# Kernel optimization log

Measured on AMD Instinct MI355X. Metric: run time of the kernel, lower is better.

## Reference

```python
import jax, jax.numpy as jnp
import numpy as np

NUM_HEADS = 12
HIDDEN = 768
HEAD_DIM = HIDDEN // NUM_HEADS  # 64
B, S = 2, 2048


def setup_inputs() -> dict:
    key = jax.random.key(0)
    ks = jax.random.split(key, 8)
    inp = {
        "hidden_states": jax.random.normal(ks[0], (B, S, HIDDEN), dtype=jnp.float32),
        "attention_mask": jnp.zeros((B, 1, 1, S), dtype=jnp.float32),
        "Wq": jax.random.normal(ks[1], (HIDDEN, HIDDEN), dtype=jnp.float32) * 0.02,
        "bq": jnp.zeros((HIDDEN,), dtype=jnp.float32),
        "Wk": jax.random.normal(ks[2], (HIDDEN, HIDDEN), dtype=jnp.float32) * 0.02,
        "bk": jnp.zeros((HIDDEN,), dtype=jnp.float32),
        "Wv": jax.random.normal(ks[3], (HIDDEN, HIDDEN), dtype=jnp.float32) * 0.02,
        "bv": jnp.zeros((HIDDEN,), dtype=jnp.float32),
    }
    return inp


def _split_heads(x):
    # [B, S, H*d] -> [B, H, S, d]
    b, s, _ = x.shape
    return x.reshape(b, s, NUM_HEADS, HEAD_DIM).transpose(0, 2, 1, 3)


def reference(hidden_states, attention_mask, Wq, bq, Wk, bk, Wv, bv):
    # Q/K/V projections (nn.Linear: x @ W.T + b; W generated square so direct matmul is equivalent math)
    q = _split_heads(hidden_states @ Wq + bq)  # [B,H,S,d]
    k = _split_heads(hidden_states @ Wk + bk)
    v = _split_heads(hidden_states @ Wv + bv)

    scale = 1.0 / np.sqrt(HEAD_DIM).astype(np.float32)
    scores = jnp.einsum("bhqd,bhkd->bhqk", q, k) * scale  # [B,H,S,S]
    scores = scores + attention_mask  # additive mask, broadcast [B,1,1,S]
    probs = jax.nn.softmax(scores, axis=-1)
    # dropout prob = 0.0 -> identity (eval mode)
    ctx = jnp.einsum("bhqk,bhkd->bhqd", probs, v)  # [B,H,S,d]
    ctx = ctx.transpose(0, 2, 1, 3).reshape(hidden_states.shape[0], hidden_states.shape[1], HIDDEN)
    return ctx
```

## Files before the change

### kernel.cpp

```cpp
#include <hip/hip_runtime.h>

#define S_LEN 2048
#define HID   768
#define NH    12
#define HD    64
#define BATCH 2
#define GK    768
#define L2E   1.44269504088896340736f
#define QSCL  (0.125f * L2E)

typedef __attribute__((ext_vector_type(8))) short bf16x8;
typedef __attribute__((ext_vector_type(4))) float f32x4;
typedef __attribute__((ext_vector_type(4))) short s16x4;
typedef __attribute__((ext_vector_type(8))) short s16x8;

__device__ __forceinline__ unsigned short f2bf(float f) {
    union { float f; unsigned int u; } v; v.f = f;
    unsigned int r = v.u + 0x7fffu + ((v.u >> 16) & 1u);
    return (unsigned short)(r >> 16);
}
__device__ __forceinline__ unsigned short f2bf_hu(float f) {
    union { float f; unsigned int u; } v; v.f = f;
    return (unsigned short)((v.u + 0x8000u) >> 16);
}

#define GLL16(gp, lp) __builtin_amdgcn_global_load_lds( \
    (const __attribute__((address_space(1))) unsigned int*)(gp), \
    (__attribute__((address_space(3))) unsigned int*)(lp), 16, 0, 0)


__global__ __launch_bounds__(256) void prep_kernel(
    const float* __restrict__ X, const float* __restrict__ Wq,
    const float* __restrict__ Wk, const float* __restrict__ Wv,
    unsigned short* __restrict__ Xb, unsigned short* __restrict__ Wt) {
    __shared__ float T[32][33];
    int bid = blockIdx.x;
    if (bid < 3072) {
        int id = bid * 256 + threadIdx.x;
        float4 v = ((const float4*)X)[id];
        s16x4 o; o[0] = (short)f2bf(v.x); o[1] = (short)f2bf(v.y);
        o[2] = (short)f2bf(v.z); o[3] = (short)f2bf(v.w);
        ((s16x4*)Xb)[id] = o;
        return;
    }
    int t2 = bid - 3072;
    int mat = t2 / 576, t = t2 % 576;
    int tk = t / 24, tn = t % 24;
    const float* W = (mat == 0) ? Wq : (mat == 1) ? Wk : Wv;
    const float scl = (mat == 0) ? QSCL : 1.0f;
    int r  = threadIdx.x >> 3;
    int c4 = (threadIdx.x & 7) * 4;
    float4 v = *(const float4*)&W[(size_t)(tk*32 + r) * GK + tn*32 + c4];
    T[c4+0][r] = v.x; T[c4+1][r] = v.y; T[c4+2][r] = v.z; T[c4+3][r] = v.w;
    __syncthreads();
    s16x4 o;
    o[0] = (short)f2bf(T[r][c4+0] * scl); o[1] = (short)f2bf(T[r][c4+1] * scl);
    o[2] = (short)f2bf(T[r][c4+2] * scl); o[3] = (short)f2bf(T[r][c4+3] * scl);
    *(s16x4*)&Wt[(size_t)(mat*768 + tn*32 + r) * GK + tk*32 + c4] = o;
}

__global__ __launch_bounds__(256) void gemm_qkv(
    const unsigned short* __restrict__ Xb, const unsigned short* __restrict__ Wt,
    const float* __restrict__ bq, const float* __restrict__ bk,
    const float* __restrict__ bv,
    unsigned short* __restrict__ qb, unsigned short* __restrict__ kb,
    unsigned short* __restrict__ vb) {
    __shared__ __align__(16) unsigned short As[2][128][64];
    __shared__ __align__(16) unsigned short Bs[2][64][64];

    const int tid = threadIdx.x;
    const int bm = blockIdx.y * 128;
    const int bn = blockIdx.x * 64;
    const int w = tid >> 6, l = tid & 63, quad = l >> 4, lq = l & 15;
    const int wx = w & 1, wy = w >> 1;

    const int srow = l >> 3, schunk = ((l & 7) ^ (l >> 3)) * 8;
    const unsigned short* aga = Xb + (size_t)(bm + w*32 + srow) * GK + schunk;
    const unsigned short* bga = Wt + (size_t)(bn + w*16 + srow) * GK + schunk;

    const int c0 = ((quad)     ^ (lq & 7)) * 8;
    const int c1 = ((4 + quad) ^ (lq & 7)) * 8;

    f32x4 zero = {0.f, 0.f, 0.f, 0.f};
    f32x4 acc[4][2];
#pragma unroll
    for (int mi = 0; mi < 4; mi++)
#pragma unroll
        for (int ni = 0; ni < 2; ni++) acc[mi][ni] = zero;

    auto stage = [&](int buf, int ks) {
        const int k0 = ks * 64;
#pragma unroll
        for (int i = 0; i < 4; i++)
            GLL16(aga + k0 + i*8*GK, &As[buf][w*32 + i*8][0]);
#pragma unroll
        for (int i = 0; i < 2; i++)
            GLL16(bga + k0 + i*8*GK, &Bs[buf][w*16 + i*8][0]);
    };

    auto compute = [&](int buf) {
#pragma unroll
        for (int kh = 0; kh < 2; kh++) {
            const int cc = kh ? c1 : c0;
            bf16x8 a[4], b[2];
#pragma unroll
            for (int mi = 0; mi < 4; mi++)
                a[mi] = *(const bf16x8*)&As[buf][wy*64 + mi*16 + lq][cc];
#pragma unroll
            for (int ni = 0; ni < 2; ni++)
                b[ni] = *(const bf16x8*)&Bs[buf][wx*32 + ni*16 + lq][cc];
#pragma unroll
            for (int mi = 0; mi < 4; mi++)
#pragma unroll
                for (int ni = 0; ni < 2; ni++)
                    acc[mi][ni] = __builtin_amdgcn_mfma_f32_16x16x32_bf16(
                        a[mi], b[ni], acc[mi][ni], 0, 0, 0);
        }
    };

    stage(0, 0);
    __syncthreads();
    for (int ks = 0; ks < GK / 64; ks += 2) {
        stage(1, ks + 1);
        compute(0);
        __syncthreads();
        if (ks + 2 < GK / 64) stage(0, ks + 2);
        compute(1);
        __syncthreads();
    }

    unsigned short* ep = (unsigned short*)As;
    const int mat = bn / 768;
    const float* bias = (mat == 0) ? bq : (mat == 1) ? bk : bv;
    const float bscl = (mat == 0) ? QSCL : 1.0f;
    const int nbase = bn % 768;
    const int h  = nbase >> 6;
    const int b_ = bm >> 11, s0 = bm & 2047;

    if (mat != 1) {
#pragma unroll
        for (int ni = 0; ni < 2; ni++) {
            int nl = wx*32 + ni*16 + lq;
            float bval = bias[nbase + nl] * bscl;
#pragma unroll
            for (int mi = 0; mi < 4; mi++) {
                int m0 = wy*64 + mi*16 + quad*4;
                s16x4 pk;
#pragma unroll
                for (int r = 0; r < 4; r++) pk[r] = (short)f2bf_hu(acc[mi][ni][r] + bval);
                *(s16x4*)&ep[nl*136 + m0] = pk;
            }
        }
        __syncthreads();
        unsigned short* outp = (mat == 0) ? qb : vb;
        unsigned short* obase = outp + ((size_t)((b_*NH + h) * HD)) * S_LEN + s0;
#pragma unroll
        for (int i = 0; i < 4; i++) {
            int id = i * 256 + tid;
            int n = id >> 4, c = id & 15;
            *(s16x8*)&obase[(size_t)n * S_LEN + c*8] = *(const s16x8*)&ep[n*136 + c*8];
        }
    } else {
#pragma unroll
        for (int ni = 0; ni < 2; ni++) {
            int nl = wx*32 + ni*16 + lq;
            float bval = bias[nbase + nl];
#pragma unroll
            for (int mi = 0; mi < 4; mi++) {
                int m0 = wy*64 + mi*16 + quad*4;
#pragma unroll
                for (int r = 0; r < 4; r++)
                    ep[(m0 + r)*66 + nl] = f2bf_hu(acc[mi][ni][r] + bval);
            }
        }
        __syncthreads();
        unsigned short* obase = kb + ((size_t)((b_*NH + h) * S_LEN + s0)) * HD;
#pragma unroll
        for (int i = 0; i < 4; i++) {
            int id = i * 256 + tid;
            int m = id >> 3, c = id & 7;
            *(s16x8*)&obase[(size_t)m * HD + c*8] = *(const s16x8*)&ep[m*66 + c*8];
        }
    }
}

__global__ __launch_bounds__(256) void attn_kernel(
    const unsigned short* __restrict__ Qtg, const unsigned short* __restrict__ Kg,
    const unsigned short* __restrict__ Vtg, const float* __restrict__ maskg,
    float* __restrict__ out) {
    __shared__ __align__(16) unsigned short Ks[2][64][64];
    __shared__ __align__(16) unsigned short Vt[2][64][64];
    __shared__ __align__(16) unsigned short Ps[4][16][72];
    __shared__ __align__(16) float mkL[S_LEN];

    const int tid = threadIdx.x;
    const int w = tid >> 6, l = tid & 63, quad = l >> 4, lq = l & 15;
    const int bh = blockIdx.y;
    const int q0 = blockIdx.x * 64;
    const int bi = bh / NH, hi = bh % NH;
    const unsigned short* Kh = Kg + (size_t)bh * S_LEN * HD;
    const unsigned short* Vh = Vtg + (size_t)bh * HD * S_LEN;

    bf16x8 a0, a1;
    {
        const unsigned short* Qt = Qtg + (size_t)bh * HD * S_LEN + (q0 + w*16 + lq);
#pragma unroll
        for (int j = 0; j < 8; j++) {
            a0[j] = (short)Qt[(size_t)(quad*8 + j) * S_LEN];
            a1[j] = (short)Qt[(size_t)(quad*8 + j + 32) * S_LEN];
        }
    }

    {
        const float4* mb4 = (const float4*)(maskg + (size_t)bi * S_LEN);
#pragma unroll
        for (int i = 0; i < 2; i++) {
            int idx = i * 256 + tid;
            float4 v = mb4[idx];
            float4 sv; sv.x = v.x*L2E; sv.y = v.y*L2E; sv.z = v.z*L2E; sv.w = v.w*L2E;
            ((float4*)mkL)[idx] = sv;
        }
    }

    bf16x8 ones;
#pragma unroll
    for (int i = 0; i < 8; i++) ones[i] = (short)0x3F80;

    const int srow = l >> 3, schunk = ((l & 7) ^ (l >> 3)) * 8;
    const unsigned short* kga = Kh + (size_t)(w*16 + srow) * HD + schunk;
    const unsigned short* vga = Vh + (size_t)(w*16 + srow) * S_LEN + schunk;

    const int c0 = ((quad)     ^ (lq & 7)) * 8;
    const int c1 = ((4 + quad) ^ (lq & 7)) * 8;

    f32x4 zero = {0.f, 0.f, 0.f, 0.f};
    f32x4 o[4], lsum = zero;
#pragma unroll
    for (int ng = 0; ng < 4; ng++) o[ng] = zero;

    auto stage = [&](int buf, int kt) {
#pragma unroll
        for (int i = 0; i < 2; i++) {
            GLL16(kga + (size_t)kt*64*HD + i*8*HD, &Ks[buf][w*16 + i*8][0]);
            GLL16(vga + kt*64 + (size_t)i*8*S_LEN, &Vt[buf][w*16 + i*8][0]);
        }
    };

    auto compute = [&](int buf, int kt) {
        const int kk = kt * 64;
        float mm[4];
#pragma unroll
        for (int g = 0; g < 4; g++) mm[g] = mkL[kk + g*16 + lq];

        f32x4 s[4];
#pragma unroll
        for (int g = 0; g < 4; g++) {
            bf16x8 b0 = *(const bf16x8*)&Ks[buf][g*16 + lq][c0];
            bf16x8 b1 = *(const bf16x8*)&Ks[buf][g*16 + lq][c1];
            f32x4 z = __builtin_amdgcn_mfma_f32_16x16x32_bf16(a0, b0, zero, 0, 0, 0);
            s[g]    = __builtin_amdgcn_mfma_f32_16x16x32_bf16(a1, b1, z,    0, 0, 0);
        }

#pragma unroll
        for (int g = 0; g < 4; g++) {
            const int col = g*16 + lq;
#pragma unroll
            for (int r = 0; r < 4; r++)
                Ps[w][quad*4 + r][col] = f2bf_hu(exp2f(s[g][r] + mm[g]));
        }

        bf16x8 pa0 = *(const bf16x8*)&Ps[w][lq][quad*8];
        bf16x8 pa1 = *(const bf16x8*)&Ps[w][lq][32 + quad*8];

        lsum = __builtin_amdgcn_mfma_f32_16x16x32_bf16(pa0, ones, lsum, 0, 0, 0);
        lsum = __builtin_amdgcn_mfma_f32_16x16x32_bf16(pa1, ones, lsum, 0, 0, 0);

#pragma unroll
        for (int ng = 0; ng < 4; ng++) {
            bf16x8 v0 = *(const bf16x8*)&Vt[buf][ng*16 + lq][c0];
            bf16x8 v1 = *(const bf16x8*)&Vt[buf][ng*16 + lq][c1];
            f32x4 t = __builtin_amdgcn_mfma_f32_16x16x32_bf16(pa0, v0, o[ng], 0, 0, 0);
            o[ng]   = __builtin_amdgcn_mfma_f32_16x16x32_bf16(pa1, v1, t,     0, 0, 0);
        }
    };

    stage(0, 0);
    __syncthreads();

    for (int kt = 0; kt < S_LEN / 64; kt += 2) {
        stage(1, kt + 1);
        compute(0, kt);
        __syncthreads();
        if (kt + 2 < S_LEN / 64) stage(0, kt + 2);
        compute(1, kt + 1);
        __syncthreads();
    }

#pragma unroll
    for (int r = 0; r < 4; r++) {
        const float inv = 1.0f / lsum[r];
        const int row = q0 + w*16 + quad*4 + r;
#pragma unroll
        for (int ng = 0; ng < 4; ng++)
            out[((size_t)(bi * S_LEN + row)) * HID + hi*HD + ng*16 + lq] = o[ng][r] * inv;
    }
}

extern "C" void kernel_launch(void* const* d_in, const int* in_sizes, int n_in,
                              void* d_out, int out_size, void* d_ws, size_t ws_size,
                              hipStream_t stream) {
    const float* X    = (const float*)d_in[0];
    const float* mask = (const float*)d_in[1];
    const float* Wq   = (const float*)d_in[2];
    const float* bq   = (const float*)d_in[3];
    const float* Wk   = (const float*)d_in[4];
    const float* bk   = (const float*)d_in[5];
    const float* Wv   = (const float*)d_in[6];
    const float* bv   = (const float*)d_in[7];
    float* out = (float*)d_out;

    const size_t per = (size_t)BATCH * NH * S_LEN * HD;
    unsigned short* qb = (unsigned short*)d_ws;
    unsigned short* kb = qb + per;
    unsigned short* vb = kb + per;
    unsigned short* xb = vb + per;
    unsigned short* wt = xb + (size_t)4096 * GK;

    prep_kernel<<<4800, 256, 0, stream>>>(X, Wq, Wk, Wv, xb, wt);

    dim3 ggrid(2304 / 64, 4096 / 128);
    gemm_qkv<<<ggrid, 256, 0, stream>>>(xb, wt, bq, bk, bv, qb, kb, vb);

    dim3 agrid(S_LEN / 64, BATCH * NH);
    attn_kernel<<<agrid, 256, 0, stream>>>(qb, kb, vb, mask, out);
}
```

Before: 162.3 us.

## Switch bf16 to fp16 MFMA with packed conversions and transpose grid order

Replaces the bf16 data path with fp16 throughout. Conversions now use hardware packed round-toward-zero cvt_pkrtz or native half casts instead of integer bit manipulation, which cuts ALU work in the prep, GEMM epilogue and softmax P-store code. Separately, both the GEMM and attention grids are transposed so that consecutive blocks walk a different dimension, changing L2 reuse of weights and K/V across concurrently scheduled blocks. fp16 has a narrower exponent range than bf16, so exp2 values or projections with large magnitude could overflow.

Result: no change. 164.2 us (+1.2%).

```diff
diff --git a/kernel.cpp b/kernel.cpp
--- a/kernel.cpp
+++ b/kernel.cpp
@@ -9,19 +9,19 @@
 #define L2E   1.44269504088896340736f
 #define QSCL  (0.125f * L2E)
 
-typedef __attribute__((ext_vector_type(8))) short bf16x8;
+typedef __attribute__((ext_vector_type(8))) _Float16 f16x8;
+typedef __attribute__((ext_vector_type(2))) __fp16 fp16v2;
 typedef __attribute__((ext_vector_type(4))) float f32x4;
 typedef __attribute__((ext_vector_type(4))) short s16x4;
 typedef __attribute__((ext_vector_type(8))) short s16x8;
 
-__device__ __forceinline__ unsigned short f2bf(float f) {
-    union { float f; unsigned int u; } v; v.f = f;
-    unsigned int r = v.u + 0x7fffu + ((v.u >> 16) & 1u);
-    return (unsigned short)(r >> 16);
-}
-__device__ __forceinline__ unsigned short f2bf_hu(float f) {
-    union { float f; unsigned int u; } v; v.f = f;
-    return (unsigned short)((v.u + 0x8000u) >> 16);
+__device__ __forceinline__ unsigned short f2h(float f) {
+    _Float16 h = (_Float16)f;
+    union { _Float16 h; unsigned short u; } v; v.h = h; return v.u;
+}
+__device__ __forceinline__ unsigned int pkh(float a, float b) {
+    fp16v2 r = __builtin_amdgcn_cvt_pkrtz(a, b);
+    union { fp16v2 h; unsigned int u; } v; v.h = r; return v.u;
 }
 
 #define GLL16(gp, lp) __builtin_amdgcn_global_load_lds( \
@@ -38,9 +38,8 @@
     if (bid < 3072) {
         int id = bid * 256 + threadIdx.x;
         float4 v = ((const float4*)X)[id];
-        s16x4 o; o[0] = (short)f2bf(v.x); o[1] = (short)f2bf(v.y);
-        o[2] = (short)f2bf(v.z); o[3] = (short)f2bf(v.w);
-        ((s16x4*)Xb)[id] = o;
+        uint2 u; u.x = pkh(v.x, v.y); u.y = pkh(v.z, v.w);
+        ((uint2*)Xb)[id] = u;
         return;
     }
     int t2 = bid - 3072;
@@ -53,10 +52,10 @@
     float4 v = *(const float4*)&W[(size_t)(tk*32 + r) * GK + tn*32 + c4];
     T[c4+0][r] = v.x; T[c4+1][r] = v.y; T[c4+2][r] = v.z; T[c4+3][r] = v.w;
     __syncthreads();
-    s16x4 o;
-    o[0] = (short)f2bf(T[r][c4+0] * scl); o[1] = (short)f2bf(T[r][c4+1] * scl);
-    o[2] = (short)f2bf(T[r][c4+2] * scl); o[3] = (short)f2bf(T[r][c4+3] * scl);
-    *(s16x4*)&Wt[(size_t)(mat*768 + tn*32 + r) * GK + tk*32 + c4] = o;
+    uint2 u;
+    u.x = pkh(T[r][c4+0] * scl, T[r][c4+1] * scl);
+    u.y = pkh(T[r][c4+2] * scl, T[r][c4+3] * scl);
+    *(uint2*)&Wt[(size_t)(mat*768 + tn*32 + r) * GK + tk*32 + c4] = u;
 }
 
 __global__ __launch_bounds__(256) void gemm_qkv(
@@ -69,8 +68,8 @@
     __shared__ __align__(16) unsigned short Bs[2][64][64];
 
     const int tid = threadIdx.x;
-    const int bm = blockIdx.y * 128;
-    const int bn = blockIdx.x * 64;
+    const int bm = blockIdx.x * 128;
+    const int bn = blockIdx.y * 64;
     const int w = tid >> 6, l = tid & 63, quad = l >> 4, lq = l & 15;
     const int wx = w & 1, wy = w >> 1;
 
@@ -102,18 +101,18 @@
 #pragma unroll
         for (int kh = 0; kh < 2; kh++) {
             const int cc = kh ? c1 : c0;
-            bf16x8 a[4], b[2];
+            f16x8 a[4], b[2];
 #pragma unroll
             for (int mi = 0; mi < 4; mi++)
-                a[mi] = *(const bf16x8*)&As[buf][wy*64 + mi*16 + lq][cc];
+                a[mi] = *(const f16x8*)&As[buf][wy*64 + mi*16 + lq][cc];
 #pragma unroll
             for (int ni = 0; ni < 2; ni++)
-                b[ni] = *(const bf16x8*)&Bs[buf][wx*32 + ni*16 + lq][cc];
+                b[ni] = *(const f16x8*)&Bs[buf][wx*32 + ni*16 + lq][cc];
 #pragma unroll
             for (int mi = 0; mi < 4; mi++)
 #pragma unroll
                 for (int ni = 0; ni < 2; ni++)
-                    acc[mi][ni] = __builtin_amdgcn_mfma_f32_16x16x32_bf16(
+                    acc[mi][ni] = __builtin_amdgcn_mfma_f32_16x16x32_f16(
                         a[mi], b[ni], acc[mi][ni], 0, 0, 0);
         }
     };
@@ -145,10 +144,10 @@
 #pragma unroll
             for (int mi = 0; mi < 4; mi++) {
                 int m0 = wy*64 + mi*16 + quad*4;
-                s16x4 pk;
-#pragma unroll
-                for (int r = 0; r < 4; r++) pk[r] = (short)f2bf_hu(acc[mi][ni][r] + bval);
-                *(s16x4*)&ep[nl*136 + m0] = pk;
+                uint2 u;
+                u.x = pkh(acc[mi][ni][0] + bval, acc[mi][ni][1] + bval);
+                u.y = pkh(acc[mi][ni][2] + bval, acc[mi][ni][3] + bval);
+                *(uint2*)&ep[nl*136 + m0] = u;
             }
         }
         __syncthreads();
@@ -170,7 +169,7 @@
                 int m0 = wy*64 + mi*16 + quad*4;
 #pragma unroll
                 for (int r = 0; r < 4; r++)
-                    ep[(m0 + r)*66 + nl] = f2bf_hu(acc[mi][ni][r] + bval);
+                    ep[(m0 + r)*66 + nl] = f2h(acc[mi][ni][r] + bval);
             }
         }
         __syncthreads();
@@ -195,21 +194,22 @@
 
     const int tid = threadIdx.x;
     const int w = tid >> 6, l = tid & 63, quad = l >> 4, lq = l & 15;
-    const int bh = blockIdx.y;
-    const int q0 = blockIdx.x * 64;
+    const int bh = blockIdx.x;
+    const int q0 = blockIdx.y * 64;
     const int bi = bh / NH, hi = bh % NH;
     const unsigned short* Kh = Kg + (size_t)bh * S_LEN * HD;
     const unsigned short* Vh = Vtg + (size_t)bh * HD * S_LEN;
 
-    bf16x8 a0, a1;
+    union { s16x8 s; f16x8 h; } ua0, ua1;
     {
         const unsigned short* Qt = Qtg + (size_t)bh * HD * S_LEN + (q0 + w*16 + lq);
 #pragma unroll
         for (int j = 0; j < 8; j++) {
-            a0[j] = (short)Qt[(size_t)(quad*8 + j) * S_LEN];
-            a1[j] = (short)Qt[(size_t)(quad*8 + j + 32) * S_LEN];
-        }
-    }
+            ua0.s[j] = (short)Qt[(size_t)(quad*8 + j) * S_LEN];
+            ua1.s[j] = (short)Qt[(size_t)(quad*8 + j + 32) * S_LEN];
+        }
+    }
+    const f16x8 a0 = ua0.h, a1 = ua1.h;
 
     {
         const float4* mb4 = (const float4*)(maskg + (size_t)bi * S_LEN);
@@ -222,9 +222,9 @@
         }
     }
 
-    bf16x8 ones;
-#pragma unroll
-    for (int i = 0; i < 8; i++) ones[i] = (short)0x3F80;
+    f16x8 ones;
+#pragma unroll
+    for (int i = 0; i < 8; i++) ones[i] = (_Float16)1.0f;
 
     const int srow = l >> 3, schunk = ((l & 7) ^ (l >> 3)) * 8;
     const unsigned short* kga = Kh + (size_t)(w*16 + srow) * HD + schunk;
@@ -255,10 +255,10 @@
         f32x4 s[4];
 #pragma unroll
         for (int g = 0; g < 4; g++) {
-            bf16x8 b0 = *(const bf16x8*)&Ks[buf][g*16 + lq][c0];
-            bf16x8 b1 = *(const bf16x8*)&Ks[buf][g*16 + lq][c1];
-            f32x4 z = __builtin_amdgcn_mfma_f32_16x16x32_bf16(a0, b0, zero, 0, 0, 0);
-            s[g]    = __builtin_amdgcn_mfma_f32_16x16x32_bf16(a1, b1, z,    0, 0, 0);
+            f16x8 b0 = *(const f16x8*)&Ks[buf][g*16 + lq][c0];
+            f16x8 b1 = *(const f16x8*)&Ks[buf][g*16 + lq][c1];
+            f32x4 z = __builtin_amdgcn_mfma_f32_16x16x32_f16(a0, b0, zero, 0, 0, 0);
+            s[g]    = __builtin_amdgcn_mfma_f32_16x16x32_f16(a1, b1, z,    0, 0, 0);
         }
 
 #pragma unroll
@@ -266,21 +266,21 @@
             const int col = g*16 + lq;
 #pragma unroll
             for (int r = 0; r < 4; r++)
-                Ps[w][quad*4 + r][col] = f2bf_hu(exp2f(s[g][r] + mm[g]));
-        }
-
-        bf16x8 pa0 = *(const bf16x8*)&Ps[w][lq][quad*8];
-        bf16x8 pa1 = *(const bf16x8*)&Ps[w][lq][32 + quad*8];
-
-        lsum = __builtin_amdgcn_mfma_f32_16x16x32_bf16(pa0, ones, lsum, 0, 0, 0);
-        lsum = __builtin_amdgcn_mfma_f32_16x16x32_bf16(pa1, ones, lsum, 0, 0, 0);
+                Ps[w][quad*4 + r][col] = f2h(exp2f(s[g][r] + mm[g]));
+        }
+
+        f16x8 pa0 = *(const f16x8*)&Ps[w][lq][quad*8];
+        f16x8 pa1 = *(const f16x8*)&Ps[w][lq][32 + quad*8];
+
+        lsum = __builtin_amdgcn_mfma_f32_16x16x32_f16(pa0, ones, lsum, 0, 0, 0);
+        lsum = __builtin_amdgcn_mfma_f32_16x16x32_f16(pa1, ones, lsum, 0, 0, 0);
 
 #pragma unroll
         for (int ng = 0; ng < 4; ng++) {
-            bf16x8 v0 = *(const bf16x8*)&Vt[buf][ng*16 + lq][c0];
-            bf16x8 v1 = *(const bf16x8*)&Vt[buf][ng*16 + lq][c1];
-            f32x4 t = __builtin_amdgcn_mfma_f32_16x16x32_bf16(pa0, v0, o[ng], 0, 0, 0);
-            o[ng]   = __builtin_amdgcn_mfma_f32_16x16x32_bf16(pa1, v1, t,     0, 0, 0);
+            f16x8 v0 = *(const f16x8*)&Vt[buf][ng*16 + lq][c0];
+            f16x8 v1 = *(const f16x8*)&Vt[buf][ng*16 + lq][c1];
+            f32x4 t = __builtin_amdgcn_mfma_f32_16x16x32_f16(pa0, v0, o[ng], 0, 0, 0);
+            o[ng]   = __builtin_amdgcn_mfma_f32_16x16x32_f16(pa1, v1, t,     0, 0, 0);
         }
     };
 
@@ -328,9 +328,9 @@
 
     prep_kernel<<<4800, 256, 0, stream>>>(X, Wq, Wk, Wv, xb, wt);
 
-    dim3 ggrid(2304 / 64, 4096 / 128);
+    dim3 ggrid(4096 / 128, 2304 / 64);
     gemm_qkv<<<ggrid, 256, 0, stream>>>(xb, wt, bq, bk, bv, qb, kb, vb);
 
-    dim3 agrid(S_LEN / 64, BATCH * NH);
+    dim3 agrid(BATCH * NH, S_LEN / 64);
     attn_kernel<<<agrid, 256, 0, stream>>>(qb, kb, vb, mask, out);
 }
```
